# Optimization experiments

Hardware: AMD Instinct MI355X
Metric: run time of the kernel (lower is better)

## Reference

```python
import jax, jax.numpy as jnp
import numpy as np

L = 7  # window size (odd)
A = 0.1
B_COEF = 0.9


def mex_hat(d):
    grid = (np.mgrid[:d, :d] - d // 2) * 1.0
    eucl = (grid ** 2).sum(0) ** 0.5
    eucl /= d
    return eucl * np.exp(-eucl)


def setup_inputs() -> dict:
    key = jax.random.key(0)
    x = jax.random.normal(key, (16, 1, 512, 512), dtype=jnp.float32)
    kernel = jnp.asarray(mex_hat(L).reshape(-1), dtype=jnp.float32)  # [49], row-major like unfold
    return {"x": x, "kernel": kernel}


def reference(x, kernel):
    # x: [B,1,H,W], kernel: [L*L]
    # Extract zero-padded LxL patches, matching F.unfold(padding=L//2) ordering
    # (C=1, kernel positions row-major). patches: [B, L*L, H, W]
    patches = jax.lax.conv_general_dilated_patches(
        x, (L, L), (1, 1), 'SAME')
    average_term = jnp.exp(-patches.mean(axis=1, keepdims=True))  # [B,1,H,W]
    differential_term = jnp.sum(
        kernel[None, :, None, None] * jax.nn.relu(patches - x),
        axis=1, keepdims=True)  # [B,1,H,W]
    suppression = A * average_term + B_COEF * differential_term
    norm = jnp.sqrt(jnp.sum(suppression ** 2))
    suppression = suppression / norm
    mask = jnp.where(x > suppression, jnp.ones_like(x), jnp.zeros_like(x))
    return mask, average_term, differential_term
```

## Files before the change

### kernel.cpp

```cpp
#include <hip/hip_runtime.h>
#include <math.h>

#define HW 512
#define NB 16
#define TX 64
#define TY 32
#define LDSW 72
#define LDSH 38
#define N_PIX (NB * HW * HW)
#define NBLK (8 * 16 * NB)

__global__ __launch_bounds__(256, 4) void li_phase1(
    const float* __restrict__ x, const float* __restrict__ kw,
    float* __restrict__ out_ratio, float* __restrict__ out_avg,
    float* __restrict__ out_dif, float* __restrict__ partials)
{
    __shared__ float tile[LDSH * LDSW];
    __shared__ float wsum[4];

    const int tid = threadIdx.x;
    const int bx = blockIdx.x, by = blockIdx.y, b = blockIdx.z;
    const int x0 = bx * TX, y0 = by * TY;
    const float* xb = x + (size_t)b * (HW * HW);

    float w[49];
#pragma unroll
    for (int i = 0; i < 49; i++) w[i] = kw[i];

    for (int idx = tid; idx < LDSH * (LDSW / 4); idx += 256) {
        int r = idx / (LDSW / 4);
        int c4 = idx - r * (LDSW / 4);
        int gy = y0 - 3 + r;
        int gx = x0 - 4 + c4 * 4;
        float4 v = make_float4(0.f, 0.f, 0.f, 0.f);
        if ((unsigned)gy < HW && (unsigned)gx < HW)
            v = *(const float4*)(xb + gy * HW + gx);
        *(float4*)&tile[r * LDSW + c4 * 4] = v;
    }
    __syncthreads();

    const int tx  = tid & 63;
    const int ty0 = (tid >> 6) * 8;

    float cen[8];
#pragma unroll
    for (int p = 0; p < 8; p++)
        cen[p] = tile[(ty0 + p + 3) * LDSW + tx + 4];

    float dif[8]  = {0, 0, 0, 0, 0, 0, 0, 0};
    float vsum[14] = {0};

#pragma unroll
    for (int dj = 0; dj < 7; dj++) {
        float c[14];
#pragma unroll
        for (int r = 0; r < 14; r++)
            c[r] = tile[(ty0 + r) * LDSW + tx + 1 + dj];
#pragma unroll
        for (int r = 0; r < 14; r++)
            vsum[r] += c[r];
#pragma unroll
        for (int r = 0; r < 14; r++) {
#pragma unroll
            for (int p = 0; p < 8; p++) {
                const int di = r - p;
                if (di >= 0 && di < 7)
                    dif[p] = fmaf(w[di * 7 + dj], fmaxf(c[r] - cen[p], 0.f), dif[p]);
            }
        }
    }

    float bsum[8];
    float s = ((vsum[0] + vsum[1]) + (vsum[2] + vsum[3])) +
              ((vsum[4] + vsum[5]) + vsum[6]);
    bsum[0] = s;
#pragma unroll
    for (int p = 1; p < 8; p++) {
        s += vsum[p + 6] - vsum[p - 1];
        bsum[p] = s;
    }

    const size_t base = (size_t)b * (HW * HW) + (size_t)(y0 + ty0) * HW + x0 + tx;
    float ss = 0.f;
#pragma unroll
    for (int p = 0; p < 8; p++) {
        float avg = __expf(-bsum[p] * (1.0f / 49.0f));
        float d = dif[p];
        float sp = 0.1f * avg + 0.9f * d;
        size_t gi = base + (size_t)p * HW;
        out_avg[gi] = avg;
        out_dif[gi] = d;
        out_ratio[gi] = cen[p] / sp;
        ss = fmaf(sp, sp, ss);
    }

#pragma unroll
    for (int off = 32; off > 0; off >>= 1)
        ss += __shfl_down(ss, off, 64);
    if ((tid & 63) == 0) wsum[tid >> 6] = ss;
    __syncthreads();
    if (tid == 0) {
        int flat = bx + 8 * (by + 16 * b);
        partials[flat] = (wsum[0] + wsum[1]) + (wsum[2] + wsum[3]);
    }
}

__global__ __launch_bounds__(256) void li_reduce(float* __restrict__ ws)
{
    __shared__ float wsum[4];
    const int tid = threadIdx.x;
    float s = 0.f;
#pragma unroll
    for (int i = 0; i < NBLK / 256; i++)
        s += ws[tid + i * 256];
#pragma unroll
    for (int off = 32; off > 0; off >>= 1)
        s += __shfl_down(s, off, 64);
    if ((tid & 63) == 0) wsum[tid >> 6] = s;
    __syncthreads();
    if (tid == 0)
        ws[NBLK] = 1.0f / sqrtf((wsum[0] + wsum[1]) + (wsum[2] + wsum[3]));
}

__global__ __launch_bounds__(256) void li_phase2(
    const float* __restrict__ ws, float* __restrict__ io)
{
    const int i = (blockIdx.x * 256 + threadIdx.x) * 4;
    const float inv = ws[NBLK];
    float4 r = *(const float4*)(io + i);
    float4 m;
    m.x = (r.x > inv) ? 1.f : 0.f;
    m.y = (r.y > inv) ? 1.f : 0.f;
    m.z = (r.z > inv) ? 1.f : 0.f;
    m.w = (r.w > inv) ? 1.f : 0.f;
    *(float4*)(io + i) = m;
}

extern "C" void kernel_launch(void* const* d_in, const int* in_sizes, int n_in,
                              void* d_out, int out_size, void* d_ws, size_t ws_size,
                              hipStream_t stream) {
    const float* x  = (const float*)d_in[0];
    const float* kw = (const float*)d_in[1];
    float* out   = (float*)d_out;
    float* ratio = out;
    float* avg   = out + N_PIX;
    float* dif   = out + 2 * (size_t)N_PIX;
    float* ws    = (float*)d_ws;

    dim3 g(HW / TX, HW / TY, NB);
    li_phase1<<<g, 256, 0, stream>>>(x, kw, ratio, avg, dif, ws);
    li_reduce<<<1, 256, 0, stream>>>(ws);
    li_phase2<<<N_PIX / 1024, 256, 0, stream>>>(ws, ratio);
}
```

Baseline: 100.8 us.

## Restructure window loop row-major, pin weights in SGPRs, raise occupancy

The 7x7 accumulation loop is reordered to walk the 14 tile rows one at a time, loading 7 columns per row and computing a row sum that is added to each affected output's box sum. This replaces the 14-entry column-sum array and sliding-window pass and lowers register pressure. Kernel weights are forced into scalar registers with readfirstlane, and launch bounds now target 8 blocks per CU. The avg and dif outputs use nontemporal stores, and the division becomes a hardware reciprocal multiply, which is slightly less precise than a true divide.

```diff
diff --git a/kernel.cpp b/kernel.cpp
--- a/kernel.cpp
+++ b/kernel.cpp
@@ -10,7 +10,11 @@
 #define N_PIX (NB * HW * HW)
 #define NBLK (8 * 16 * NB)
 
-__global__ __launch_bounds__(256, 4) void li_phase1(
+__device__ __forceinline__ float sgpr_f(float v) {
+    return __uint_as_float(__builtin_amdgcn_readfirstlane(__float_as_uint(v)));
+}
+
+__global__ __launch_bounds__(256, 8) void li_phase1(
     const float* __restrict__ x, const float* __restrict__ kw,
     float* __restrict__ out_ratio, float* __restrict__ out_avg,
     float* __restrict__ out_dif, float* __restrict__ partials)
@@ -25,7 +29,7 @@
 
     float w[49];
 #pragma unroll
-    for (int i = 0; i < 49; i++) w[i] = kw[i];
+    for (int i = 0; i < 49; i++) w[i] = sgpr_f(kw[i]);
 
     for (int idx = tid; idx < LDSH * (LDSW / 4); idx += 256) {
         int r = idx / (LDSW / 4);
@@ -48,36 +52,26 @@
         cen[p] = tile[(ty0 + p + 3) * LDSW + tx + 4];
 
     float dif[8]  = {0, 0, 0, 0, 0, 0, 0, 0};
-    float vsum[14] = {0};
+    float bsum[8] = {0, 0, 0, 0, 0, 0, 0, 0};
 
 #pragma unroll
-    for (int dj = 0; dj < 7; dj++) {
-        float c[14];
+    for (int r = 0; r < 14; r++) {
+        float v[7];
 #pragma unroll
-        for (int r = 0; r < 14; r++)
-            c[r] = tile[(ty0 + r) * LDSW + tx + 1 + dj];
+        for (int dj = 0; dj < 7; dj++)
+            v[dj] = tile[(ty0 + r) * LDSW + tx + 1 + dj];
+
+        float rs = ((v[0] + v[1]) + (v[2] + v[3])) + ((v[4] + v[5]) + v[6]);
 #pragma unroll
-        for (int r = 0; r < 14; r++)
-            vsum[r] += c[r];
+        for (int p = 0; p < 8; p++) {
+            const int di = r - p;
+            if (di >= 0 && di < 7) {
+                bsum[p] += rs;
 #pragma unroll
-        for (int r = 0; r < 14; r++) {
-#pragma unroll
-            for (int p = 0; p < 8; p++) {
-                const int di = r - p;
-                if (di >= 0 && di < 7)
-                    dif[p] = fmaf(w[di * 7 + dj], fmaxf(c[r] - cen[p], 0.f), dif[p]);
+                for (int dj = 0; dj < 7; dj++)
+                    dif[p] = fmaf(w[di * 7 + dj], fmaxf(v[dj] - cen[p], 0.f), dif[p]);
             }
         }
-    }
-
-    float bsum[8];
-    float s = ((vsum[0] + vsum[1]) + (vsum[2] + vsum[3])) +
-              ((vsum[4] + vsum[5]) + vsum[6]);
-    bsum[0] = s;
-#pragma unroll
-    for (int p = 1; p < 8; p++) {
-        s += vsum[p + 6] - vsum[p - 1];
-        bsum[p] = s;
     }
 
     const size_t base = (size_t)b * (HW * HW) + (size_t)(y0 + ty0) * HW + x0 + tx;
@@ -88,9 +82,9 @@
         float d = dif[p];
         float sp = 0.1f * avg + 0.9f * d;
         size_t gi = base + (size_t)p * HW;
-        out_avg[gi] = avg;
-        out_dif[gi] = d;
-        out_ratio[gi] = cen[p] / sp;
+        __builtin_nontemporal_store(avg, out_avg + gi);
+        __builtin_nontemporal_store(d,   out_dif + gi);
+        out_ratio[gi] = cen[p] * __builtin_amdgcn_rcpf(sp);
         ss = fmaf(sp, sp, ss);
     }
 
```

New measurement: 97.24 us. 1.04x faster.
